# Optimization experiments

Hardware: AMD Instinct MI355X
Metric: run time of the kernel (lower is better)

Reference implementation:

```python
import jax, jax.numpy as jnp
import numpy as np

D_MODEL = 1024
D_INNER = 2048   # d_model * expansion_factor(2)
D_CONV = 4
N_EXPERTS = 8
TOP_K = 2


def setup_inputs() -> dict:
    key = jax.random.key(0)
    ks = jax.random.split(key, 6)
    s = 0.02
    return {
        "x": jax.random.normal(ks[0], (4, 2048, D_MODEL), jnp.float32),
        "Wr": jax.random.normal(ks[1], (N_EXPERTS, D_MODEL), jnp.float32) * s,
        "br": jnp.zeros((N_EXPERTS,), jnp.float32),
        "Win": jax.random.normal(ks[2], (N_EXPERTS, 2 * D_INNER, D_MODEL), jnp.float32) * s,
        "conv_w": jax.random.normal(ks[3], (N_EXPERTS, D_INNER, D_CONV), jnp.float32) * s,
        "conv_b": jnp.zeros((N_EXPERTS, D_INNER), jnp.float32),
        "Dp": jnp.ones((N_EXPERTS, D_INNER), jnp.float32),
        "Wout": jax.random.normal(ks[4], (N_EXPERTS, D_MODEL, D_INNER), jnp.float32) * s,
    }


def reference(x, Wr, br, Win, conv_w, conv_b, Dp, Wout):
    B, L, C = x.shape
    xf = x.reshape(-1, C)                                   # [N, C]
    logits = xf @ Wr.T + br                                 # [N, E]
    probs = jax.nn.softmax(logits.astype(jnp.float32), axis=-1)
    tw, ti = jax.lax.top_k(probs, TOP_K)                    # [N, k]
    tw = tw / jnp.sum(tw, axis=-1, keepdims=True)
    oh = jax.nn.one_hot(ti, N_EXPERTS, dtype=jnp.float32)   # [N, k, E]
    load = oh.sum(1).mean(0)                                # [E]
    aux_loss = jnp.sum(load * load)
    # per-token combine weight for each expert (sum over top-k slots)
    cw = jnp.einsum('nk,nke->ne', tw, oh)                   # [N, E]
    out = jnp.zeros_like(xf)
    for j in range(N_EXPERTS):
        # Per-token expert (L=1 inside the original loop): causal depthwise
        # conv with left padding reduces to last-tap * x + bias.
        xz = xf @ Win[j].T                                  # [N, 2*D_INNER]
        xi, z = xz[:, :D_INNER], xz[:, D_INNER:]
        xa = jax.nn.silu(xi * conv_w[j, :, -1] + conv_b[j])
        y = xa * Dp[j] * jax.nn.silu(z)
        out = out + cw[:, j:j + 1].astype(xf.dtype) * (y @ Wout[j].T)
    return out.reshape(B, L, C), aux_loss
```

## Files before the change

kernel.cpp:

```cpp
#include <hip/hip_runtime.h>
#include <hip/hip_bf16.h>
#include <stdint.h>

#define NTOK 8192
#define CDIM 1024
#define DIN  2048
#define NEXP 8
#define NSLOT (NTOK * 2)

typedef __bf16 bf16x8 __attribute__((ext_vector_type(8)));
typedef float  f32x4  __attribute__((ext_vector_type(4)));

typedef __attribute__((address_space(1))) const unsigned char GBUF;
typedef __attribute__((address_space(3))) unsigned char LBUF;

__device__ __forceinline__ void gload_lds16(const void* g, void* l) {
    __builtin_amdgcn_global_load_lds((GBUF*)g, (LBUF*)l, 16, 0, 0);
}

__device__ __forceinline__ ushort f2bf(float f) {
    union { float f; unsigned u; } v; v.f = f;
    unsigned u = v.u;
    u += 0x7fffu + ((u >> 16) & 1u);
    return (ushort)(u >> 16);
}
__device__ __forceinline__ float bf2f(ushort u) {
    union { float f; unsigned u; } v; v.u = ((unsigned)u) << 16; return v.f;
}
__device__ __forceinline__ float silu_f(float x) { return x / (1.f + __expf(-x)); }

__device__ __forceinline__ bf16x8 lds_swz(const ushort* L, int row, int kof) {
    return *(const bf16x8*)&L[row * 64 + ((((kof >> 3) ^ row) & 7) << 3)];
}

#define WAITV(N) asm volatile("s_waitcnt vmcnt(" #N ")" ::: "memory")
#define BARR     __builtin_amdgcn_s_barrier()

__global__ void __launch_bounds__(256) k_cvt2(
    const float* __restrict__ srcA, ushort* __restrict__ dstA, int nA4,
    const float* __restrict__ srcB, ushort* __restrict__ dstB, int nB4) {
    int i = blockIdx.x * 256 + threadIdx.x;
    int stride = gridDim.x * 256;
    int ntot = nA4 + nB4;
    for (; i < ntot; i += stride) {
        const float4* s; ushort4* d; int j;
        if (i < nA4) { s = (const float4*)srcA; d = (ushort4*)dstA; j = i; }
        else         { s = (const float4*)srcB; d = (ushort4*)dstB; j = i - nA4; }
        float4 v = s[j];
        ushort4 o;
        o.x = f2bf(v.x); o.y = f2bf(v.y); o.z = f2bf(v.z); o.w = f2bf(v.w);
        d[j] = o;
    }
}

__global__ void __launch_bounds__(256) k_router(
    const float* __restrict__ x, const float* __restrict__ Wr,
    const float* __restrict__ br, int* __restrict__ counts,
    int* __restrict__ tok_e, float* __restrict__ tok_w,
    ushort* __restrict__ xb) {
    int wave = blockIdx.x * 4 + (threadIdx.x >> 6);
    int lane = threadIdx.x & 63;
    const float4* row = (const float4*)(x + (size_t)wave * CDIM);
    ushort4* xrow = (ushort4*)(xb + (size_t)wave * CDIM);
    float acc[NEXP];
#pragma unroll
    for (int e = 0; e < NEXP; ++e) acc[e] = 0.f;
#pragma unroll
    for (int j = 0; j < 4; ++j) {
        float4 v = row[j * 64 + lane];
        ushort4 o;
        o.x = f2bf(v.x); o.y = f2bf(v.y); o.z = f2bf(v.z); o.w = f2bf(v.w);
        xrow[j * 64 + lane] = o;
#pragma unroll
        for (int e = 0; e < NEXP; ++e) {
            float4 w = ((const float4*)(Wr + e * CDIM))[j * 64 + lane];
            acc[e] += v.x * w.x + v.y * w.y + v.z * w.z + v.w * w.w;
        }
    }
#pragma unroll
    for (int off = 32; off > 0; off >>= 1)
#pragma unroll
        for (int e = 0; e < NEXP; ++e) acc[e] += __shfl_xor(acc[e], off, 64);
    if (lane == 0) {
        float l[NEXP];
#pragma unroll
        for (int e = 0; e < NEXP; ++e) l[e] = acc[e] + br[e];
        int i0 = 0; float l0 = l[0];
#pragma unroll
        for (int e = 1; e < NEXP; ++e) if (l[e] > l0) { l0 = l[e]; i0 = e; }
        int i1 = -1; float l1 = -1e30f;
#pragma unroll
        for (int e = 0; e < NEXP; ++e) if (e != i0 && l[e] > l1) { l1 = l[e]; i1 = e; }
        float s  = __expf(l1 - l0);
        float w0 = 1.f / (1.f + s);
        float w1 = 1.f - w0;
        tok_e[wave * 2] = i0; tok_e[wave * 2 + 1] = i1;
        tok_w[wave * 2] = w0; tok_w[wave * 2 + 1] = w1;
        atomicAdd(&counts[i0], 1); atomicAdd(&counts[i1], 1);
    }
}

__global__ void __launch_bounds__(256) k_scatter(
    const int* __restrict__ tok_e, const int* __restrict__ counts,
    int* __restrict__ cursor, int* __restrict__ perm_token,
    int* __restrict__ tok_slot, float* __restrict__ out_aux) {
    int t = blockIdx.x * 256 + threadIdx.x;
    if (t >= NTOK) return;
    if (t == 0) {
        float aux = 0.f;
#pragma unroll
        for (int k = 0; k < NEXP; ++k) {
            float ld = (float)counts[k] * (1.f / (float)NTOK);
            aux += ld * ld;
        }
        *out_aux = aux;
    }
#pragma unroll
    for (int k = 0; k < 2; ++k) {
        int e = tok_e[t * 2 + k];
        int off = 0, o = 0;
#pragma unroll
        for (int j = 0; j < NEXP; ++j) {
            if (j == e) off = o;
            o += counts[j];
        }
        int pos = atomicAdd(&cursor[e], 1);
        int s = off + pos;
        perm_token[s] = t;
        tok_slot[t * 2 + k] = s;
    }
}

__global__ void __launch_bounds__(512, 2) k_gemm1(
    const ushort* __restrict__ xb, const ushort* __restrict__ Winb,
    const float* __restrict__ conv_w, const float* __restrict__ conv_b,
    const float* __restrict__ Dp, const int* __restrict__ counts,
    const int* __restrict__ perm_token, ushort* __restrict__ y) {
    int h = blockIdx.x;
    int vb = (h & 7) * 160 + (h >> 3);
    int e   = vb / 160;
    int r   = vb % 160;
    int mt0 = r >> 4;
    int nt  = r & 15;
    int base = 0;
#pragma unroll
    for (int k = 0; k < NEXP; ++k) if (k < e) base += counts[k];
    int cnt = counts[e];
    if (cnt == 0) return;
    int mtiles = (cnt + 255) >> 8;
    int n0 = nt * 128;

    __shared__ ushort aL[2][256 * 64];
    __shared__ ushort bL[2][256 * 64];

    int tid = threadIdx.x, lane = tid & 63, w = tid >> 6;
    int Mw = w >> 1, Nw = w & 1;
    const ushort* WinE = Winb + (size_t)e * (2 * DIN) * CDIM;
    int schunk = ((tid & 7) ^ ((tid >> 3) & 7)) << 3;

    uint bsrc[4];
#pragma unroll
    for (int i = 0; i < 4; ++i) {
        int rr = i * 64 + (tid >> 3);
        int grow = (rr < 128) ? (n0 + rr) : (DIN + n0 + (rr - 128));
        bsrc[i] = (uint)grow * CDIM + schunk;
    }

    for (int mt = mt0; mt < mtiles; mt += 10) {
        int rem = cnt - mt * 256;
        uint asrc[4];
#pragma unroll
        for (int i = 0; i < 4; ++i) {
            int rr = i * 64 + (tid >> 3);
            int sidx = base + mt * 256 + (rr < rem ? rr : 0);
            asrc[i] = (uint)perm_token[sidx] * CDIM + schunk;
        }

        f32x4 accXi[4][4], accZ[4][4];
#pragma unroll
        for (int m = 0; m < 4; ++m)
#pragma unroll
            for (int n = 0; n < 4; ++n) {
                accXi[m][n] = f32x4{0.f, 0.f, 0.f, 0.f};
                accZ[m][n]  = f32x4{0.f, 0.f, 0.f, 0.f};
            }

        auto stgA = [&](int bi, int ko, int i, int j) {
            gload_lds16(xb + asrc[i] + ko, &aL[bi][(i * 512 + tid) * 8]);
            gload_lds16(xb + asrc[j] + ko, &aL[bi][(j * 512 + tid) * 8]);
        };
        auto stgB = [&](int bi, int ko, int i, int j) {
            gload_lds16(WinE + bsrc[i] + ko, &bL[bi][(i * 512 + tid) * 8]);
            gload_lds16(WinE + bsrc[j] + ko, &bL[bi][(j * 512 + tid) * 8]);
        };

        bf16x8 af0[4], af1[4], bx[4], bz[4];
        stgA(0, 0, 0, 1); stgA(0, 0, 2, 3); stgB(0, 0, 0, 1); stgB(0, 0, 2, 3);

#pragma unroll 1
        for (int kt = 0; kt < 16; ++kt) {
            int cur = kt & 1, nxt = cur ^ 1;
            const ushort* A = aL[cur];
            const ushort* B = bL[cur];
            int ko = (kt + 1) * 64;
            bool st = kt < 15;
            WAITV(2);
            BARR;
#pragma unroll
            for (int m = 0; m < 4; ++m)
                af0[m] = lds_swz(A, Mw * 64 + m * 16 + (lane & 15), (lane >> 4) * 8);
#pragma unroll
            for (int n = 0; n < 4; ++n)
                bx[n] = lds_swz(B, Nw * 64 + n * 16 + (lane & 15), (lane >> 4) * 8);
            if (st) stgA(nxt, ko, 0, 1);
            __builtin_amdgcn_s_setprio(1);
#pragma unroll
            for (int m = 0; m < 4; ++m)
#pragma unroll
                for (int n = 0; n < 4; ++n)
                    accXi[m][n] = __builtin_amdgcn_mfma_f32_16x16x32_bf16(af0[m], bx[n], accXi[m][n], 0, 0, 0);
            __builtin_amdgcn_s_setprio(0);
            if (st) { WAITV(2); } else { WAITV(0); }
            BARR;
#pragma unroll
            for (int n = 0; n < 4; ++n)
                bz[n] = lds_swz(B, 128 + Nw * 64 + n * 16 + (lane & 15), (lane >> 4) * 8);
            if (st) stgA(nxt, ko, 2, 3);
            __builtin_amdgcn_s_setprio(1);
#pragma unroll
            for (int m = 0; m < 4; ++m)
#pragma unroll
                for (int n = 0; n < 4; ++n)
                    accZ[m][n] = __builtin_amdgcn_mfma_f32_16x16x32_bf16(af0[m], bz[n], accZ[m][n], 0, 0, 0);
            __builtin_amdgcn_s_setprio(0);
            BARR;
#pragma unroll
            for (int m = 0; m < 4; ++m)
                af1[m] = lds_swz(A, Mw * 64 + m * 16 + (lane & 15), 32 + (lane >> 4) * 8);
#pragma unroll
            for (int n = 0; n < 4; ++n)
                bx[n] = lds_swz(B, Nw * 64 + n * 16 + (lane & 15), 32 + (lane >> 4) * 8);
            if (st) stgB(nxt, ko, 0, 1);
            __builtin_amdgcn_s_setprio(1);
#pragma unroll
            for (int m = 0; m < 4; ++m)
#pragma unroll
                for (int n = 0; n < 4; ++n)
                    accXi[m][n] = __builtin_amdgcn_mfma_f32_16x16x32_bf16(af1[m], bx[n], accXi[m][n], 0, 0, 0);
            __builtin_amdgcn_s_setprio(0);
            BARR;
#pragma unroll
            for (int n = 0; n < 4; ++n)
                bz[n] = lds_swz(B, 128 + Nw * 64 + n * 16 + (lane & 15), 32 + (lane >> 4) * 8);
            if (st) stgB(nxt, ko, 2, 3);
            __builtin_amdgcn_s_setprio(1);
#pragma unroll
            for (int m = 0; m < 4; ++m)
#pragma unroll
                for (int n = 0; n < 4; ++n)
                    accZ[m][n] = __builtin_amdgcn_mfma_f32_16x16x32_bf16(af1[m], bz[n], accZ[m][n], 0, 0, 0);
            __builtin_amdgcn_s_setprio(0);
        }
        __syncthreads();

#pragma unroll
        for (int n = 0; n < 4; ++n) {
            int c = n0 + Nw * 64 + n * 16 + (lane & 15);
            float cwl = conv_w[((size_t)e * DIN + c) * 4 + 3];
            float cb  = conv_b[(size_t)e * DIN + c];
            float dp  = Dp[(size_t)e * DIN + c];
#pragma unroll
            for (int m = 0; m < 4; ++m)
#pragma unroll
                for (int q = 0; q < 4; ++q) {
                    int rl = Mw * 64 + m * 16 + (lane >> 4) * 4 + q;
                    if (rl < rem) {
                        int slot = base + mt * 256 + rl;
                        float xi = accXi[m][n][q], z = accZ[m][n][q];
                        float yv = silu_f(xi * cwl + cb) * dp * silu_f(z);
                        y[(size_t)slot * DIN + c] = f2bf(yv);
                    }
                }
        }
        __syncthreads();
    }
}

__global__ void __launch_bounds__(512, 4) k_gemm2(
    const ushort* __restrict__ y, const ushort* __restrict__ Woutb,
    const int* __restrict__ counts, ushort* __restrict__ so) {
    __shared__ ushort aL[256 * 64];
    __shared__ ushort bL[128 * 64];

    int tid = threadIdx.x, lane = tid & 63, w = tid >> 6;
    int Mw = w >> 1, Nw = w & 1;
    int schunk = ((tid & 7) ^ ((tid >> 3) & 7)) << 3;

    int c0_, c1_, c2_, c3_, c4_, c5_, c6_, c7_;
    c0_ = counts[0]; c1_ = counts[1]; c2_ = counts[2]; c3_ = counts[3];
    c4_ = counts[4]; c5_ = counts[5]; c6_ = counts[6]; c7_ = counts[7];
    int cn[NEXP] = {c0_, c1_, c2_, c3_, c4_, c5_, c6_, c7_};
    int tot_mtiles = 0;
#pragma unroll
    for (int k = 0; k < NEXP; ++k) tot_mtiles += (cn[k] + 255) >> 8;
    int ntiles = tot_mtiles * 8;
    int b = blockIdx.x;
    int virt = (b & 7) * 64 + (b >> 3);

    for (int t = virt; t < ntiles; t += 512) {
        int pair = t >> 3, nt = t & 7;
        int e = 0, mt = pair, base = 0, cnt = cn[0];
        {
            int o = 0, tp = 0;
#pragma unroll
            for (int k = 0; k < NEXP; ++k) {
                int ck = cn[k];
                int tk = (ck + 255) >> 8;
                if (pair >= tp) { e = k; mt = pair - tp; base = o; cnt = ck; }
                o += ck; tp += tk;
            }
        }
        int rem = cnt - mt * 256;
        int c0 = nt * 128;
        const ushort* WoutE = Woutb + (size_t)e * CDIM * DIN;

        uint asrc[4], bsrc[2];
#pragma unroll
        for (int i = 0; i < 4; ++i) {
            int rr = i * 64 + (tid >> 3);
            int slot = base + mt * 256 + (rr < rem ? rr : 0);
            asrc[i] = (uint)slot * DIN + schunk;
        }
#pragma unroll
        for (int i = 0; i < 2; ++i) {
            int rr = i * 64 + (tid >> 3);
            bsrc[i] = (uint)(c0 + rr) * DIN + schunk;
        }

        f32x4 acc[4][4];
#pragma unroll
        for (int m = 0; m < 4; ++m)
#pragma unroll
            for (int n = 0; n < 4; ++n) acc[m][n] = f32x4{0.f, 0.f, 0.f, 0.f};

#pragma unroll 1
        for (int kt = 0; kt < 32; ++kt) {
            int ko = kt * 64;
            gload_lds16(y + asrc[0] + ko, &aL[(0 * 512 + tid) * 8]);
            gload_lds16(y + asrc[1] + ko, &aL[(1 * 512 + tid) * 8]);
            gload_lds16(y + asrc[2] + ko, &aL[(2 * 512 + tid) * 8]);
            gload_lds16(y + asrc[3] + ko, &aL[(3 * 512 + tid) * 8]);
            gload_lds16(WoutE + bsrc[0] + ko, &bL[(0 * 512 + tid) * 8]);
            gload_lds16(WoutE + bsrc[1] + ko, &bL[(1 * 512 + tid) * 8]);
            __syncthreads();
#pragma unroll
            for (int kk = 0; kk < 64; kk += 32) {
                int kof = kk + (lane >> 4) * 8;
                bf16x8 af[4], bf[4];
#pragma unroll
                for (int m = 0; m < 4; ++m)
                    af[m] = lds_swz(aL, Mw * 64 + m * 16 + (lane & 15), kof);
#pragma unroll
                for (int n = 0; n < 4; ++n)
                    bf[n] = lds_swz(bL, Nw * 64 + n * 16 + (lane & 15), kof);
                __builtin_amdgcn_s_setprio(1);
#pragma unroll
                for (int m = 0; m < 4; ++m)
#pragma unroll
                    for (int n = 0; n < 4; ++n)
                        acc[m][n] = __builtin_amdgcn_mfma_f32_16x16x32_bf16(af[m], bf[n], acc[m][n], 0, 0, 0);
                __builtin_amdgcn_s_setprio(0);
            }
            __syncthreads();
        }

#pragma unroll
        for (int m = 0; m < 4; ++m)
#pragma unroll
            for (int q = 0; q < 4; ++q) {
                int rl = Mw * 64 + m * 16 + (lane >> 4) * 4 + q;
                if (rl < rem) {
                    int slot = base + mt * 256 + rl;
#pragma unroll
                    for (int n = 0; n < 4; ++n) {
                        int col = c0 + Nw * 64 + n * 16 + (lane & 15);
                        so[(size_t)slot * CDIM + col] = f2bf(acc[m][n][q]);
                    }
                }
            }
        __syncthreads();
    }
}

__global__ void __launch_bounds__(256) k_combine(
    const ushort* __restrict__ so, const int* __restrict__ tok_slot,
    const float* __restrict__ tok_w, float* __restrict__ out) {
    int i = blockIdx.x * 256 + threadIdx.x;
    int t  = i >> 7;
    int c8 = (i & 127) << 3;
    int s0 = tok_slot[t * 2], s1 = tok_slot[t * 2 + 1];
    float w0 = tok_w[t * 2],  w1 = tok_w[t * 2 + 1];
    uint4 a = *(const uint4*)(so + (size_t)s0 * CDIM + c8);
    uint4 b = *(const uint4*)(so + (size_t)s1 * CDIM + c8);
    const ushort* au = (const ushort*)&a;
    const ushort* bu = (const ushort*)&b;
    float4 o0, o1;
    o0.x = w0 * bf2f(au[0]) + w1 * bf2f(bu[0]);
    o0.y = w0 * bf2f(au[1]) + w1 * bf2f(bu[1]);
    o0.z = w0 * bf2f(au[2]) + w1 * bf2f(bu[2]);
    o0.w = w0 * bf2f(au[3]) + w1 * bf2f(bu[3]);
    o1.x = w0 * bf2f(au[4]) + w1 * bf2f(bu[4]);
    o1.y = w0 * bf2f(au[5]) + w1 * bf2f(bu[5]);
    o1.z = w0 * bf2f(au[6]) + w1 * bf2f(bu[6]);
    o1.w = w0 * bf2f(au[7]) + w1 * bf2f(bu[7]);
    float4* dst = (float4*)(out + (size_t)t * CDIM + c8);
    dst[0] = o0; dst[1] = o1;
}

extern "C" void kernel_launch(void* const* d_in, const int* in_sizes, int n_in,
                              void* d_out, int out_size, void* d_ws, size_t ws_size,
                              hipStream_t stream) {
    const float* x      = (const float*)d_in[0];
    const float* Wr     = (const float*)d_in[1];
    const float* br     = (const float*)d_in[2];
    const float* Win    = (const float*)d_in[3];
    const float* conv_w = (const float*)d_in[4];
    const float* conv_b = (const float*)d_in[5];
    const float* Dp     = (const float*)d_in[6];
    const float* Wout   = (const float*)d_in[7];
    float* out = (float*)d_out;

    char* ws = (char*)d_ws;
    int*    counts     = (int*)(ws + 0);
    int*    cursor     = (int*)(ws + 128);
    int*    tok_e      = (int*)(ws + 4096);
    float*  tok_w      = (float*)(ws + 4096 + 1 * 65536);
    int*    perm_token = (int*)(ws + 4096 + 2 * 65536);
    int*    tok_slot   = (int*)(ws + 4096 + 3 * 65536);
    const size_t MB = 1u << 20;
    ushort* y     = (ushort*)(ws + MB);
    ushort* xb    = (ushort*)(ws + MB + 67108864);
    ushort* winb  = (ushort*)(ws + MB + 67108864 + 16777216);
    ushort* woutb = (ushort*)(ws + MB + 67108864 + 16777216 + 67108864);
    ushort* so    = winb;

    hipMemsetAsync(ws, 0, 256, stream);

    k_cvt2<<<3072, 256, 0, stream>>>(Win,  winb,  NEXP * 2 * DIN * CDIM / 4,
                                     Wout, woutb, NEXP * CDIM * DIN / 4);

    k_router<<<NTOK / 4, 256, 0, stream>>>(x, Wr, br, counts, tok_e, tok_w, xb);
    k_scatter<<<NTOK / 256, 256, 0, stream>>>(tok_e, counts, cursor, perm_token,
                                              tok_slot, out + (size_t)NTOK * CDIM);

    k_gemm1<<<NEXP * 160, 512, 0, stream>>>(xb, winb, conv_w, conv_b, Dp,
                                            counts, perm_token, y);
    k_gemm2<<<512, 512, 0, stream>>>(y, woutb, counts, so);
    k_combine<<<NTOK * 128 / 256, 256, 0, stream>>>(so, tok_slot, tok_w, out);
}
```

Baseline: 620.9 us.

## Retile gemm1 to persistent flattened tiles and fuse weight conversion with router

Merges the weight bf16-conversion kernel and the router into one launch so both run concurrently and one kernel launch is dropped. gemm1 moves from a fixed per-expert grid of 256x128-wide tiles (with a hand-interleaved 64-deep K pipeline) to a persistent 512-block grid over flattened (expert, m-tile, n-tile) work. Each tile is now 256x64 per half with a 32-deep K step and a simple double-buffered stage/compute loop. Smaller LDS footprint allows 4 blocks per CU. The intent is better load balance and occupancy, at the cost of less operand reuse per tile and more barriers per K step.

Measured after the change: 631.9 us. Within noise of the previous version (+1.8%).

```diff
diff --git a/kernel.cpp b/kernel.cpp
--- a/kernel.cpp
+++ b/kernel.cpp
@@ -33,32 +33,31 @@
     return *(const bf16x8*)&L[row * 64 + ((((kof >> 3) ^ row) & 7) << 3)];
 }
 
-#define WAITV(N) asm volatile("s_waitcnt vmcnt(" #N ")" ::: "memory")
-#define BARR     __builtin_amdgcn_s_barrier()
-
-__global__ void __launch_bounds__(256) k_cvt2(
-    const float* __restrict__ srcA, ushort* __restrict__ dstA, int nA4,
-    const float* __restrict__ srcB, ushort* __restrict__ dstB, int nB4) {
-    int i = blockIdx.x * 256 + threadIdx.x;
-    int stride = gridDim.x * 256;
-    int ntot = nA4 + nB4;
-    for (; i < ntot; i += stride) {
-        const float4* s; ushort4* d; int j;
-        if (i < nA4) { s = (const float4*)srcA; d = (ushort4*)dstA; j = i; }
-        else         { s = (const float4*)srcB; d = (ushort4*)dstB; j = i - nA4; }
-        float4 v = s[j];
-        ushort4 o;
-        o.x = f2bf(v.x); o.y = f2bf(v.y); o.z = f2bf(v.z); o.w = f2bf(v.w);
-        d[j] = o;
-    }
-}
-
-__global__ void __launch_bounds__(256) k_router(
+__global__ void __launch_bounds__(256) k_prep(
+    const float* __restrict__ Win, ushort* __restrict__ winb,
+    const float* __restrict__ Wout, ushort* __restrict__ woutb,
     const float* __restrict__ x, const float* __restrict__ Wr,
     const float* __restrict__ br, int* __restrict__ counts,
     int* __restrict__ tok_e, float* __restrict__ tok_w,
     ushort* __restrict__ xb) {
-    int wave = blockIdx.x * 4 + (threadIdx.x >> 6);
+    if (blockIdx.x < 3072) {
+        const int nA4 = NEXP * 2 * DIN * CDIM / 4;
+        const int nB4 = NEXP * CDIM * DIN / 4;
+        int i = blockIdx.x * 256 + threadIdx.x;
+        int stride = 3072 * 256;
+        int ntot = nA4 + nB4;
+        for (; i < ntot; i += stride) {
+            const float4* s; ushort4* d; int j;
+            if (i < nA4) { s = (const float4*)Win;  d = (ushort4*)winb;  j = i; }
+            else         { s = (const float4*)Wout; d = (ushort4*)woutb; j = i - nA4; }
+            float4 v = s[j];
+            ushort4 o;
+            o.x = f2bf(v.x); o.y = f2bf(v.y); o.z = f2bf(v.z); o.w = f2bf(v.w);
+            d[j] = o;
+        }
+        return;
+    }
+    int wave = (blockIdx.x - 3072) * 4 + (threadIdx.x >> 6);
     int lane = threadIdx.x & 63;
     const float4* row = (const float4*)(x + (size_t)wave * CDIM);
     ushort4* xrow = (ushort4*)(xb + (size_t)wave * CDIM);
@@ -131,141 +130,113 @@
     }
 }
 
-__global__ void __launch_bounds__(512, 2) k_gemm1(
+__global__ void __launch_bounds__(512, 4) k_gemm1(
     const ushort* __restrict__ xb, const ushort* __restrict__ Winb,
     const float* __restrict__ conv_w, const float* __restrict__ conv_b,
     const float* __restrict__ Dp, const int* __restrict__ counts,
     const int* __restrict__ perm_token, ushort* __restrict__ y) {
-    int h = blockIdx.x;
-    int vb = (h & 7) * 160 + (h >> 3);
-    int e   = vb / 160;
-    int r   = vb % 160;
-    int mt0 = r >> 4;
-    int nt  = r & 15;
-    int base = 0;
-#pragma unroll
-    for (int k = 0; k < NEXP; ++k) if (k < e) base += counts[k];
-    int cnt = counts[e];
-    if (cnt == 0) return;
-    int mtiles = (cnt + 255) >> 8;
-    int n0 = nt * 128;
-
-    __shared__ ushort aL[2][256 * 64];
-    __shared__ ushort bL[2][256 * 64];
+    __shared__ ushort aL[2][256 * 32];
+    __shared__ ushort bL[2][128 * 32];
 
     int tid = threadIdx.x, lane = tid & 63, w = tid >> 6;
     int Mw = w >> 1, Nw = w & 1;
-    const ushort* WinE = Winb + (size_t)e * (2 * DIN) * CDIM;
-    int schunk = ((tid & 7) ^ ((tid >> 3) & 7)) << 3;
-
-    uint bsrc[4];
-#pragma unroll
-    for (int i = 0; i < 4; ++i) {
-        int rr = i * 64 + (tid >> 3);
-        int grow = (rr < 128) ? (n0 + rr) : (DIN + n0 + (rr - 128));
-        bsrc[i] = (uint)grow * CDIM + schunk;
-    }
-
-    for (int mt = mt0; mt < mtiles; mt += 10) {
+
+    int cn[NEXP];
+#pragma unroll
+    for (int k = 0; k < NEXP; ++k) cn[k] = counts[k];
+    int tot_mtiles = 0;
+#pragma unroll
+    for (int k = 0; k < NEXP; ++k) tot_mtiles += (cn[k] + 255) >> 8;
+    int ntiles = tot_mtiles * 32;
+    int b = blockIdx.x;
+    int virt = (b & 7) * 64 + (b >> 3);
+
+    int arow0 = tid >> 2;
+    int arow1 = 128 + arow0;
+    int ac    = tid & 3;
+    int acol0 = ((ac ^ ((arow0 >> 1) & 3)) << 3);
+    int acol1 = ((ac ^ ((arow1 >> 1) & 3)) << 3);
+    int brow  = tid >> 2;
+    int bcol  = ((ac ^ ((brow >> 1) & 3)) << 3);
+
+    for (int t = virt; t < ntiles; t += 512) {
+        int pair = t >> 5, nt = t & 31;
+        int e = 0, mt = pair, base = 0, cnt = cn[0];
+        {
+            int o = 0, tp = 0;
+#pragma unroll
+            for (int k = 0; k < NEXP; ++k) {
+                int ck = cn[k];
+                int tk = (ck + 255) >> 8;
+                if (pair >= tp) { e = k; mt = pair - tp; base = o; cnt = ck; }
+                o += ck; tp += tk;
+            }
+        }
         int rem = cnt - mt * 256;
-        uint asrc[4];
-#pragma unroll
-        for (int i = 0; i < 4; ++i) {
-            int rr = i * 64 + (tid >> 3);
-            int sidx = base + mt * 256 + (rr < rem ? rr : 0);
-            asrc[i] = (uint)perm_token[sidx] * CDIM + schunk;
-        }
-
-        f32x4 accXi[4][4], accZ[4][4];
+        int n0 = nt * 64;
+        const ushort* WinE = Winb + (size_t)e * (2 * DIN) * CDIM;
+
+        uint asrc0 = (uint)perm_token[base + mt * 256 + (arow0 < rem ? arow0 : 0)] * CDIM + acol0;
+        uint asrc1 = (uint)perm_token[base + mt * 256 + (arow1 < rem ? arow1 : 0)] * CDIM + acol1;
+        int  grow  = (brow < 64) ? (n0 + brow) : (DIN + n0 + (brow - 64));
+        uint bsrc  = (uint)grow * CDIM + bcol;
+
+        f32x4 accXi[4][2], accZ[4][2];
 #pragma unroll
         for (int m = 0; m < 4; ++m)
 #pragma unroll
-            for (int n = 0; n < 4; ++n) {
+            for (int n = 0; n < 2; ++n) {
                 accXi[m][n] = f32x4{0.f, 0.f, 0.f, 0.f};
                 accZ[m][n]  = f32x4{0.f, 0.f, 0.f, 0.f};
             }
 
-        auto stgA = [&](int bi, int ko, int i, int j) {
-            gload_lds16(xb + asrc[i] + ko, &aL[bi][(i * 512 + tid) * 8]);
-            gload_lds16(xb + asrc[j] + ko, &aL[bi][(j * 512 + tid) * 8]);
+        auto stage = [&](int bi, int kc) {
+            int ko = kc * 32;
+            gload_lds16(xb   + asrc0 + ko, &aL[bi][tid * 8]);
+            gload_lds16(xb   + asrc1 + ko, &aL[bi][(512 + tid) * 8]);
+            gload_lds16(WinE + bsrc  + ko, &bL[bi][tid * 8]);
         };
-        auto stgB = [&](int bi, int ko, int i, int j) {
-            gload_lds16(WinE + bsrc[i] + ko, &bL[bi][(i * 512 + tid) * 8]);
-            gload_lds16(WinE + bsrc[j] + ko, &bL[bi][(j * 512 + tid) * 8]);
+        auto compute = [&](int bi) {
+            const ushort* A = aL[bi];
+            const ushort* B = bL[bi];
+            bf16x8 af[4], bx[2], bz[2];
+#pragma unroll
+            for (int m = 0; m < 4; ++m) {
+                int ra = Mw * 64 + m * 16 + (lane & 15);
+                int k4 = (lane >> 4) ^ ((ra >> 1) & 3);
+                af[m] = *(const bf16x8*)&A[ra * 32 + k4 * 8];
+            }
+#pragma unroll
+            for (int n = 0; n < 2; ++n) {
+                int rb = Nw * 32 + n * 16 + (lane & 15);
+                int k4 = (lane >> 4) ^ ((rb >> 1) & 3);
+                bx[n] = *(const bf16x8*)&B[rb * 32 + k4 * 8];
+                bz[n] = *(const bf16x8*)&B[(64 + rb) * 32 + k4 * 8];
+            }
+            __builtin_amdgcn_s_setprio(1);
+#pragma unroll
+            for (int m = 0; m < 4; ++m)
+#pragma unroll
+                for (int n = 0; n < 2; ++n) {
+                    accXi[m][n] = __builtin_amdgcn_mfma_f32_16x16x32_bf16(af[m], bx[n], accXi[m][n], 0, 0, 0);
+                    accZ[m][n]  = __builtin_amdgcn_mfma_f32_16x16x32_bf16(af[m], bz[n],  accZ[m][n],  0, 0, 0);
+                }
+            __builtin_amdgcn_s_setprio(0);
         };
 
-        bf16x8 af0[4], af1[4], bx[4], bz[4];
-        stgA(0, 0, 0, 1); stgA(0, 0, 2, 3); stgB(0, 0, 0, 1); stgB(0, 0, 2, 3);
-
-#pragma unroll 1
-        for (int kt = 0; kt < 16; ++kt) {
-            int cur = kt & 1, nxt = cur ^ 1;
-            const ushort* A = aL[cur];
-            const ushort* B = bL[cur];
-            int ko = (kt + 1) * 64;
-            bool st = kt < 15;
-            WAITV(2);
-            BARR;
-#pragma unroll
-            for (int m = 0; m < 4; ++m)
-                af0[m] = lds_swz(A, Mw * 64 + m * 16 + (lane & 15), (lane >> 4) * 8);
-#pragma unroll
-            for (int n = 0; n < 4; ++n)
-                bx[n] = lds_swz(B, Nw * 64 + n * 16 + (lane & 15), (lane >> 4) * 8);
-            if (st) stgA(nxt, ko, 0, 1);
-            __builtin_amdgcn_s_setprio(1);
-#pragma unroll
-            for (int m = 0; m < 4; ++m)
-#pragma unroll
-                for (int n = 0; n < 4; ++n)
-                    accXi[m][n] = __builtin_amdgcn_mfma_f32_16x16x32_bf16(af0[m], bx[n], accXi[m][n], 0, 0, 0);
-            __builtin_amdgcn_s_setprio(0);
-            if (st) { WAITV(2); } else { WAITV(0); }
-            BARR;
-#pragma unroll
-            for (int n = 0; n < 4; ++n)
-                bz[n] = lds_swz(B, 128 + Nw * 64 + n * 16 + (lane & 15), (lane >> 4) * 8);
-            if (st) stgA(nxt, ko, 2, 3);
-            __builtin_amdgcn_s_setprio(1);
-#pragma unroll
-            for (int m = 0; m < 4; ++m)
-#pragma unroll
-                for (int n = 0; n < 4; ++n)
-                    accZ[m][n] = __builtin_amdgcn_mfma_f32_16x16x32_bf16(af0[m], bz[n], accZ[m][n], 0, 0, 0);
-            __builtin_amdgcn_s_setprio(0);
-            BARR;
-#pragma unroll
-            for (int m = 0; m < 4; ++m)
-                af1[m] = lds_swz(A, Mw * 64 + m * 16 + (lane & 15), 32 + (lane >> 4) * 8);
-#pragma unroll
-            for (int n = 0; n < 4; ++n)
-                bx[n] = lds_swz(B, Nw * 64 + n * 16 + (lane & 15), 32 + (lane >> 4) * 8);
-            if (st) stgB(nxt, ko, 0, 1);
-            __builtin_amdgcn_s_setprio(1);
-#pragma unroll
-            for (int m = 0; m < 4; ++m)
-#pragma unroll
-                for (int n = 0; n < 4; ++n)
-                    accXi[m][n] = __builtin_amdgcn_mfma_f32_16x16x32_bf16(af1[m], bx[n], accXi[m][n], 0, 0, 0);
-            __builtin_amdgcn_s_setprio(0);
-            BARR;
-#pragma unroll
-            for (int n = 0; n < 4; ++n)
-                bz[n] = lds_swz(B, 128 + Nw * 64 + n * 16 + (lane & 15), 32 + (lane >> 4) * 8);
-            if (st) stgB(nxt, ko, 2, 3);
-            __builtin_amdgcn_s_setprio(1);
-#pragma unroll
-            for (int m = 0; m < 4; ++m)
-#pragma unroll
-                for (int n = 0; n < 4; ++n)
-                    accZ[m][n] = __builtin_amdgcn_mfma_f32_16x16x32_bf16(af1[m], bz[n], accZ[m][n], 0, 0, 0);
-            __builtin_amdgcn_s_setprio(0);
-        }
+        stage(0, 0);
         __syncthreads();
-
-#pragma unroll
-        for (int n = 0; n < 4; ++n) {
-            int c = n0 + Nw * 64 + n * 16 + (lane & 15);
+#pragma unroll 2
+        for (int kc = 0; kc < 32; ++kc) {
+            int cur = kc & 1;
+            if (kc < 31) stage(cur ^ 1, kc + 1);
+            compute(cur);
+            __syncthreads();
+        }
+
+#pragma unroll
+        for (int n = 0; n < 2; ++n) {
+            int c = n0 + Nw * 32 + n * 16 + (lane & 15);
             float cwl = conv_w[((size_t)e * DIN + c) * 4 + 3];
             float cb  = conv_b[(size_t)e * DIN + c];
             float dp  = Dp[(size_t)e * DIN + c];
@@ -296,10 +267,9 @@
     int Mw = w >> 1, Nw = w & 1;
     int schunk = ((tid & 7) ^ ((tid >> 3) & 7)) << 3;
 
-    int c0_, c1_, c2_, c3_, c4_, c5_, c6_, c7_;
-    c0_ = counts[0]; c1_ = counts[1]; c2_ = counts[2]; c3_ = counts[3];
-    c4_ = counts[4]; c5_ = counts[5]; c6_ = counts[6]; c7_ = counts[7];
-    int cn[NEXP] = {c0_, c1_, c2_, c3_, c4_, c5_, c6_, c7_};
+    int cn[NEXP];
+#pragma unroll
+    for (int k = 0; k < NEXP; ++k) cn[k] = counts[k];
     int tot_mtiles = 0;
 #pragma unroll
     for (int k = 0; k < NEXP; ++k) tot_mtiles += (cn[k] + 255) >> 8;
@@ -446,15 +416,13 @@
 
     hipMemsetAsync(ws, 0, 256, stream);
 
-    k_cvt2<<<3072, 256, 0, stream>>>(Win,  winb,  NEXP * 2 * DIN * CDIM / 4,
-                                     Wout, woutb, NEXP * CDIM * DIN / 4);
-
-    k_router<<<NTOK / 4, 256, 0, stream>>>(x, Wr, br, counts, tok_e, tok_w, xb);
+    k_prep<<<5120, 256, 0, stream>>>(Win, winb, Wout, woutb,
+                                     x, Wr, br, counts, tok_e, tok_w, xb);
     k_scatter<<<NTOK / 256, 256, 0, stream>>>(tok_e, counts, cursor, perm_token,
                                               tok_slot, out + (size_t)NTOK * CDIM);
 
-    k_gemm1<<<NEXP * 160, 512, 0, stream>>>(xb, winb, conv_w, conv_b, Dp,
-                                            counts, perm_token, y);
+    k_gemm1<<<512, 512, 0, stream>>>(xb, winb, conv_w, conv_b, Dp,
+                                     counts, perm_token, y);
     k_gemm2<<<512, 512, 0, stream>>>(y, woutb, counts, so);
     k_combine<<<NTOK * 128 / 256, 256, 0, stream>>>(so, tok_slot, tok_w, out);
 }
```

## Fuse fp32-to-bf16 weight conversion into expert GEMM B-tile loads

Applied to the files above, without the earlier changes.

Drops the separate kernel that converted Win and Wout to bf16 on every call. The GEMMs now read fp32 weights directly into registers, pack them to bf16 and write them to swizzled LDS. This saves a full read and write pass over both weight tensors. In exchange, weight tiles re-read by several m-tiles now move twice the bytes, register-staged loads replace async LDS loads, and gemm1's interleaved barrier pipeline is simplified to one sync per k-step.

Result: slower. 898.0 us (+44.6%).

```diff
diff --git a/kernel.cpp b/kernel.cpp
--- a/kernel.cpp
+++ b/kernel.cpp
@@ -18,39 +18,29 @@
     __builtin_amdgcn_global_load_lds((GBUF*)g, (LBUF*)l, 16, 0, 0);
 }
 
-__device__ __forceinline__ ushort f2bf(float f) {
+__device__ __forceinline__ unsigned f2bf1(float f) {
     union { float f; unsigned u; } v; v.f = f;
     unsigned u = v.u;
     u += 0x7fffu + ((u >> 16) & 1u);
-    return (ushort)(u >> 16);
-}
+    return u >> 16;
+}
+__device__ __forceinline__ ushort f2bf(float f) { return (ushort)f2bf1(f); }
 __device__ __forceinline__ float bf2f(ushort u) {
     union { float f; unsigned u; } v; v.u = ((unsigned)u) << 16; return v.f;
 }
 __device__ __forceinline__ float silu_f(float x) { return x / (1.f + __expf(-x)); }
 
+__device__ __forceinline__ uint4 pack8(float4 a, float4 b) {
+    uint4 o;
+    o.x = f2bf1(a.x) | (f2bf1(a.y) << 16);
+    o.y = f2bf1(a.z) | (f2bf1(a.w) << 16);
+    o.z = f2bf1(b.x) | (f2bf1(b.y) << 16);
+    o.w = f2bf1(b.z) | (f2bf1(b.w) << 16);
+    return o;
+}
+
 __device__ __forceinline__ bf16x8 lds_swz(const ushort* L, int row, int kof) {
     return *(const bf16x8*)&L[row * 64 + ((((kof >> 3) ^ row) & 7) << 3)];
-}
-
-#define WAITV(N) asm volatile("s_waitcnt vmcnt(" #N ")" ::: "memory")
-#define BARR     __builtin_amdgcn_s_barrier()
-
-__global__ void __launch_bounds__(256) k_cvt2(
-    const float* __restrict__ srcA, ushort* __restrict__ dstA, int nA4,
-    const float* __restrict__ srcB, ushort* __restrict__ dstB, int nB4) {
-    int i = blockIdx.x * 256 + threadIdx.x;
-    int stride = gridDim.x * 256;
-    int ntot = nA4 + nB4;
-    for (; i < ntot; i += stride) {
-        const float4* s; ushort4* d; int j;
-        if (i < nA4) { s = (const float4*)srcA; d = (ushort4*)dstA; j = i; }
-        else         { s = (const float4*)srcB; d = (ushort4*)dstB; j = i - nA4; }
-        float4 v = s[j];
-        ushort4 o;
-        o.x = f2bf(v.x); o.y = f2bf(v.y); o.z = f2bf(v.z); o.w = f2bf(v.w);
-        d[j] = o;
-    }
 }
 
 __global__ void __launch_bounds__(256) k_router(
@@ -132,7 +122,7 @@
 }
 
 __global__ void __launch_bounds__(512, 2) k_gemm1(
-    const ushort* __restrict__ xb, const ushort* __restrict__ Winb,
+    const ushort* __restrict__ xb, const float* __restrict__ Win,
     const float* __restrict__ conv_w, const float* __restrict__ conv_b,
     const float* __restrict__ Dp, const int* __restrict__ counts,
     const int* __restrict__ perm_token, ushort* __restrict__ y) {
@@ -155,15 +145,18 @@
 
     int tid = threadIdx.x, lane = tid & 63, w = tid >> 6;
     int Mw = w >> 1, Nw = w & 1;
-    const ushort* WinE = Winb + (size_t)e * (2 * DIN) * CDIM;
+    const float* WinE = Win + (size_t)e * (2 * DIN) * CDIM;
     int schunk = ((tid & 7) ^ ((tid >> 3) & 7)) << 3;
 
-    uint bsrc[4];
-#pragma unroll
-    for (int i = 0; i < 4; ++i) {
-        int rr = i * 64 + (tid >> 3);
-        int grow = (rr < 128) ? (n0 + rr) : (DIN + n0 + (rr - 128));
-        bsrc[i] = (uint)grow * CDIM + schunk;
+    int brow = tid >> 1;
+    int bcb  = (tid & 1) * 32;
+    int bgrow = (brow < 128) ? (n0 + brow) : (DIN + n0 + (brow - 128));
+    uint bsrc = (uint)bgrow * CDIM + bcb;
+    uint bdst[4];
+#pragma unroll
+    for (int w2 = 0; w2 < 4; ++w2) {
+        int jc = (tid & 1) * 4 + w2;
+        bdst[w2] = brow * 64 + ((jc ^ (brow & 7)) << 3);
     }
 
     for (int mt = mt0; mt < mtiles; mt += 10) {
@@ -185,83 +178,65 @@
                 accZ[m][n]  = f32x4{0.f, 0.f, 0.f, 0.f};
             }
 
-        auto stgA = [&](int bi, int ko, int i, int j) {
-            gload_lds16(xb + asrc[i] + ko, &aL[bi][(i * 512 + tid) * 8]);
-            gload_lds16(xb + asrc[j] + ko, &aL[bi][(j * 512 + tid) * 8]);
+        float4 v[8];
+        auto loadB = [&](int ko) {
+            const float4* s = (const float4*)(WinE + bsrc + ko);
+#pragma unroll
+            for (int u = 0; u < 8; ++u) v[u] = s[u];
         };
-        auto stgB = [&](int bi, int ko, int i, int j) {
-            gload_lds16(WinE + bsrc[i] + ko, &bL[bi][(i * 512 + tid) * 8]);
-            gload_lds16(WinE + bsrc[j] + ko, &bL[bi][(j * 512 + tid) * 8]);
+        auto writeB = [&](int bi) {
+#pragma unroll
+            for (int w2 = 0; w2 < 4; ++w2)
+                *(uint4*)&bL[bi][bdst[w2]] = pack8(v[2 * w2], v[2 * w2 + 1]);
         };
-
-        bf16x8 af0[4], af1[4], bx[4], bz[4];
-        stgA(0, 0, 0, 1); stgA(0, 0, 2, 3); stgB(0, 0, 0, 1); stgB(0, 0, 2, 3);
-
-#pragma unroll 1
+        auto stgA = [&](int bi, int ko) {
+            gload_lds16(xb + asrc[0] + ko, &aL[bi][(0 * 512 + tid) * 8]);
+            gload_lds16(xb + asrc[1] + ko, &aL[bi][(1 * 512 + tid) * 8]);
+            gload_lds16(xb + asrc[2] + ko, &aL[bi][(2 * 512 + tid) * 8]);
+            gload_lds16(xb + asrc[3] + ko, &aL[bi][(3 * 512 + tid) * 8]);
+        };
+        auto compute = [&](int bi) {
+            const ushort* A = aL[bi];
+            const ushort* B = bL[bi];
+#pragma unroll
+            for (int kk = 0; kk < 64; kk += 32) {
+                int kof = kk + (lane >> 4) * 8;
+                bf16x8 af[4], bx[4], bz[4];
+#pragma unroll
+                for (int m = 0; m < 4; ++m)
+                    af[m] = lds_swz(A, Mw * 64 + m * 16 + (lane & 15), kof);
+#pragma unroll
+                for (int n = 0; n < 4; ++n) {
+                    int cl = Nw * 64 + n * 16 + (lane & 15);
+                    bx[n] = lds_swz(B, cl, kof);
+                    bz[n] = lds_swz(B, 128 + cl, kof);
+                }
+                __builtin_amdgcn_s_setprio(1);
+#pragma unroll
+                for (int m = 0; m < 4; ++m)
+#pragma unroll
+                    for (int n = 0; n < 4; ++n) {
+                        accXi[m][n] = __builtin_amdgcn_mfma_f32_16x16x32_bf16(af[m], bx[n], accXi[m][n], 0, 0, 0);
+                        accZ[m][n]  = __builtin_amdgcn_mfma_f32_16x16x32_bf16(af[m], bz[n],  accZ[m][n],  0, 0, 0);
+                    }
+                __builtin_amdgcn_s_setprio(0);
+            }
+        };
+
+        loadB(0);
+        stgA(0, 0);
+        writeB(0);
+        __syncthreads();
+#pragma unroll 2
         for (int kt = 0; kt < 16; ++kt) {
             int cur = kt & 1, nxt = cur ^ 1;
-            const ushort* A = aL[cur];
-            const ushort* B = bL[cur];
+            bool st = kt < 15;
             int ko = (kt + 1) * 64;
-            bool st = kt < 15;
-            WAITV(2);
-            BARR;
-#pragma unroll
-            for (int m = 0; m < 4; ++m)
-                af0[m] = lds_swz(A, Mw * 64 + m * 16 + (lane & 15), (lane >> 4) * 8);
-#pragma unroll
-            for (int n = 0; n < 4; ++n)
-                bx[n] = lds_swz(B, Nw * 64 + n * 16 + (lane & 15), (lane >> 4) * 8);
-            if (st) stgA(nxt, ko, 0, 1);
-            __builtin_amdgcn_s_setprio(1);
-#pragma unroll
-            for (int m = 0; m < 4; ++m)
-#pragma unroll
-                for (int n = 0; n < 4; ++n)
-                    accXi[m][n] = __builtin_amdgcn_mfma_f32_16x16x32_bf16(af0[m], bx[n], accXi[m][n], 0, 0, 0);
-            __builtin_amdgcn_s_setprio(0);
-            if (st) { WAITV(2); } else { WAITV(0); }
-            BARR;
-#pragma unroll
-            for (int n = 0; n < 4; ++n)
-                bz[n] = lds_swz(B, 128 + Nw * 64 + n * 16 + (lane & 15), (lane >> 4) * 8);
-            if (st) stgA(nxt, ko, 2, 3);
-            __builtin_amdgcn_s_setprio(1);
-#pragma unroll
-            for (int m = 0; m < 4; ++m)
-#pragma unroll
-                for (int n = 0; n < 4; ++n)
-                    accZ[m][n] = __builtin_amdgcn_mfma_f32_16x16x32_bf16(af0[m], bz[n], accZ[m][n], 0, 0, 0);
-            __builtin_amdgcn_s_setprio(0);
-            BARR;
-#pragma unroll
-            for (int m = 0; m < 4; ++m)
-                af1[m] = lds_swz(A, Mw * 64 + m * 16 + (lane & 15), 32 + (lane >> 4) * 8);
-#pragma unroll
-            for (int n = 0; n < 4; ++n)
-                bx[n] = lds_swz(B, Nw * 64 + n * 16 + (lane & 15), 32 + (lane >> 4) * 8);
-            if (st) stgB(nxt, ko, 0, 1);
-            __builtin_amdgcn_s_setprio(1);
-#pragma unroll
-            for (int m = 0; m < 4; ++m)
-#pragma unroll
-                for (int n = 0; n < 4; ++n)
-                    accXi[m][n] = __builtin_amdgcn_mfma_f32_16x16x32_bf16(af1[m], bx[n], accXi[m][n], 0, 0, 0);
-            __builtin_amdgcn_s_setprio(0);
-            BARR;
-#pragma unroll
-            for (int n = 0; n < 4; ++n)
-                bz[n] = lds_swz(B, 128 + Nw * 64 + n * 16 + (lane & 15), 32 + (lane >> 4) * 8);
-            if (st) stgB(nxt, ko, 2, 3);
-            __builtin_amdgcn_s_setprio(1);
-#pragma unroll
-            for (int m = 0; m < 4; ++m)
-#pragma unroll
-                for (int n = 0; n < 4; ++n)
-                    accZ[m][n] = __builtin_amdgcn_mfma_f32_16x16x32_bf16(af1[m], bz[n], accZ[m][n], 0, 0, 0);
-            __builtin_amdgcn_s_setprio(0);
-        }
-        __syncthreads();
+            if (st) { loadB(ko); stgA(nxt, ko); }
+            compute(cur);
+            if (st) writeB(nxt);
+            __syncthreads();
+        }
 
 #pragma unroll
         for (int n = 0; n < 4; ++n) {
@@ -287,7 +262,7 @@
 }
 
 __global__ void __launch_bounds__(512, 4) k_gemm2(
-    const ushort* __restrict__ y, const ushort* __restrict__ Woutb,
+    const ushort* __restrict__ y, const float* __restrict__ Wout,
     const int* __restrict__ counts, ushort* __restrict__ so) {
     __shared__ ushort aL[256 * 64];
     __shared__ ushort bL[128 * 64];
@@ -296,16 +271,24 @@
     int Mw = w >> 1, Nw = w & 1;
     int schunk = ((tid & 7) ^ ((tid >> 3) & 7)) << 3;
 
-    int c0_, c1_, c2_, c3_, c4_, c5_, c6_, c7_;
-    c0_ = counts[0]; c1_ = counts[1]; c2_ = counts[2]; c3_ = counts[3];
-    c4_ = counts[4]; c5_ = counts[5]; c6_ = counts[6]; c7_ = counts[7];
-    int cn[NEXP] = {c0_, c1_, c2_, c3_, c4_, c5_, c6_, c7_};
+    int cn[NEXP];
+#pragma unroll
+    for (int k = 0; k < NEXP; ++k) cn[k] = counts[k];
     int tot_mtiles = 0;
 #pragma unroll
     for (int k = 0; k < NEXP; ++k) tot_mtiles += (cn[k] + 255) >> 8;
     int ntiles = tot_mtiles * 8;
     int b = blockIdx.x;
     int virt = (b & 7) * 64 + (b >> 3);
+
+    int brow = tid >> 2;
+    int bcb  = (tid & 3) * 16;
+    uint bdst[2];
+#pragma unroll
+    for (int w2 = 0; w2 < 2; ++w2) {
+        int jc = (tid & 3) * 2 + w2;
+        bdst[w2] = brow * 64 + ((jc ^ (brow & 7)) << 3);
+    }
 
     for (int t = virt; t < ntiles; t += 512) {
         int pair = t >> 3, nt = t & 7;
@@ -322,20 +305,16 @@
         }
         int rem = cnt - mt * 256;
         int c0 = nt * 128;
-        const ushort* WoutE = Woutb + (size_t)e * CDIM * DIN;
-
-        uint asrc[4], bsrc[2];
+        const float* WoutE = Wout + (size_t)e * CDIM * DIN;
+        uint bsrc = (uint)(c0 + brow) * DIN + bcb;
+
+        uint asrc[4];
 #pragma unroll
         for (int i = 0; i < 4; ++i) {
             int rr = i * 64 + (tid >> 3);
             int slot = base + mt * 256 + (rr < rem ? rr : 0);
             asrc[i] = (uint)slot * DIN + schunk;
         }
-#pragma unroll
-        for (int i = 0; i < 2; ++i) {
-            int rr = i * 64 + (tid >> 3);
-            bsrc[i] = (uint)(c0 + rr) * DIN + schunk;
-        }
 
         f32x4 acc[4][4];
 #pragma unroll
@@ -346,12 +325,17 @@
 #pragma unroll 1
         for (int kt = 0; kt < 32; ++kt) {
             int ko = kt * 64;
+            float4 v[4];
+            const float4* s = (const float4*)(WoutE + bsrc + ko);
+#pragma unroll
+            for (int u = 0; u < 4; ++u) v[u] = s[u];
             gload_lds16(y + asrc[0] + ko, &aL[(0 * 512 + tid) * 8]);
             gload_lds16(y + asrc[1] + ko, &aL[(1 * 512 + tid) * 8]);
             gload_lds16(y + asrc[2] + ko, &aL[(2 * 512 + tid) * 8]);
             gload_lds16(y + asrc[3] + ko, &aL[(3 * 512 + tid) * 8]);
-            gload_lds16(WoutE + bsrc[0] + ko, &bL[(0 * 512 + tid) * 8]);
-            gload_lds16(WoutE + bsrc[1] + ko, &bL[(1 * 512 + tid) * 8]);
+#pragma unroll
+            for (int w2 = 0; w2 < 2; ++w2)
+                *(uint4*)&bL[bdst[w2]] = pack8(v[2 * w2], v[2 * w2 + 1]);
             __syncthreads();
 #pragma unroll
             for (int kk = 0; kk < 64; kk += 32) {
@@ -438,23 +422,18 @@
     int*    perm_token = (int*)(ws + 4096 + 2 * 65536);
     int*    tok_slot   = (int*)(ws + 4096 + 3 * 65536);
     const size_t MB = 1u << 20;
-    ushort* y     = (ushort*)(ws + MB);
-    ushort* xb    = (ushort*)(ws + MB + 67108864);
-    ushort* winb  = (ushort*)(ws + MB + 67108864 + 16777216);
-    ushort* woutb = (ushort*)(ws + MB + 67108864 + 16777216 + 67108864);
-    ushort* so    = winb;
+    ushort* y  = (ushort*)(ws + MB);
+    ushort* xb = (ushort*)(ws + MB + 67108864);
+    ushort* so = (ushort*)(ws + MB + 67108864 + 16777216);
 
     hipMemsetAsync(ws, 0, 256, stream);
-
-    k_cvt2<<<3072, 256, 0, stream>>>(Win,  winb,  NEXP * 2 * DIN * CDIM / 4,
-                                     Wout, woutb, NEXP * CDIM * DIN / 4);
 
     k_router<<<NTOK / 4, 256, 0, stream>>>(x, Wr, br, counts, tok_e, tok_w, xb);
     k_scatter<<<NTOK / 256, 256, 0, stream>>>(tok_e, counts, cursor, perm_token,
                                               tok_slot, out + (size_t)NTOK * CDIM);
 
-    k_gemm1<<<NEXP * 160, 512, 0, stream>>>(xb, winb, conv_w, conv_b, Dp,
+    k_gemm1<<<NEXP * 160, 512, 0, stream>>>(xb, Win, conv_w, conv_b, Dp,
                                             counts, perm_token, y);
-    k_gemm2<<<512, 512, 0, stream>>>(y, woutb, counts, so);
+    k_gemm2<<<512, 512, 0, stream>>>(y, Wout, counts, so);
     k_combine<<<NTOK * 128 / 256, 256, 0, stream>>>(so, tok_slot, tok_w, out);
 }
```
